# Optimization experiments

Hardware: AMD Instinct MI355X
Metric: run time of the kernel (lower is better)

## Reference

```python
import jax, jax.numpy as jnp
import numpy as np

B, T, C, H = 4, 4096, 1024, 16
HD = C // H  # 64


def setup_inputs() -> dict:
    key = jax.random.key(0)
    k1, k2, k3, k4 = jax.random.split(key, 4)
    x = jax.random.normal(k1, (B, T, C), dtype=jnp.float32)
    Wqkv = jax.random.normal(k2, (3 * C, C), dtype=jnp.float32) * (1.0 / np.sqrt(C))
    Wout = jax.random.normal(k3, (C, C), dtype=jnp.float32) * (1.0 / np.sqrt(C))
    bout = jax.random.normal(k4, (C,), dtype=jnp.float32) * 0.02
    return {"x": x, "Wqkv": Wqkv, "Wout": Wout, "bout": bout}


def reference(x, Wqkv, Wout, bout):
    # qkv projection (torch Linear: y = x @ W.T)
    qkv = x @ Wqkv.T                              # (B, T, 3C)
    qkv = qkv.reshape(B, T, H, 3 * HD)            # view(B, T, heads, 3*head_dim)
    q, k, v = jnp.split(qkv, 3, axis=-1)          # each (B, T, H, HD)
    # NOTE: faithful to source: q @ k.transpose(-2,-1) batches over (B,T)
    # and contracts head_dim -> attention over the HEADS axis, shape (B,T,H,H).
    att = jnp.einsum("bthd,btgd->bthg", q, k) / np.float32(np.sqrt(HD))
    att = jax.nn.softmax(att, axis=-1)            # softmax over heads axis g
    out = jnp.einsum("bthg,btgd->bthd", att, v)   # (B, T, H, HD)
    out = out.reshape(B, T, C)
    return out @ Wout.T + bout
```

## Files before the change

kernel.cpp:

```cpp
#include <hip/hip_runtime.h>
#include <hip/hip_bf16.h>
#include <stdint.h>

typedef __attribute__((ext_vector_type(8))) short bf16x8;
typedef __attribute__((ext_vector_type(4))) float f32x4;

__device__ __forceinline__ float b2f(unsigned short u) {
  union { unsigned u32; float f; } c; c.u32 = ((unsigned)u) << 16; return c.f;
}
__device__ __forceinline__ unsigned short f2b(float f) {
  union { float f; unsigned u; } c; c.f = f;
  unsigned u = c.u;
  return (unsigned short)((u + 0x7FFFu + ((u >> 16) & 1u)) >> 16);
}

__global__ __launch_bounds__(256) void cast_f32_bf16(const float* __restrict__ in,
                                                     unsigned short* __restrict__ out,
                                                     int n8) {
  int i = blockIdx.x * 256 + threadIdx.x;
  if (i >= n8) return;
  const float4* p = (const float4*)in + (size_t)i * 2;
  float4 a = p[0], b = p[1];
  union { bf16x8 v; unsigned short s[8]; } o;
  o.s[0] = f2b(a.x); o.s[1] = f2b(a.y); o.s[2] = f2b(a.z); o.s[3] = f2b(a.w);
  o.s[4] = f2b(b.x); o.s[5] = f2b(b.y); o.s[6] = f2b(b.z); o.s[7] = f2b(b.w);
  ((bf16x8*)out)[i] = o.v;
}

#define GLDS16(g, l)                                                          \
  __builtin_amdgcn_global_load_lds((const __attribute__((address_space(1))) void*)(g), \
                                   (__attribute__((address_space(3))) void*)(l), 16, 0, 0)

template <typename OutT, bool BIAS>
__global__ __launch_bounds__(256) void gemm_bt(const unsigned short* __restrict__ A,
                                               const unsigned short* __restrict__ B,
                                               OutT* __restrict__ C,
                                               const float* __restrict__ bias,
                                               int M, int N, int K) {
  __shared__ unsigned short As[128 * 32];
  __shared__ unsigned short Bs[128 * 32];
  const int tid  = threadIdx.x;
  const int lane = tid & 63;
  const int wave = tid >> 6;
  const int tileM = blockIdx.y * 128;
  const int tileN = blockIdx.x * 128;

  const int m_off = (wave >> 1) * 64;
  const int n_off = (wave & 1) * 64;

  f32x4 acc[4][4] = {};

  const int srow = tid >> 2;
  const int scol = (tid & 3) * 8;
  const unsigned short* gA = A + (size_t)(tileM + srow) * K + scol;
  const unsigned short* gB = B + (size_t)(tileN + srow) * K + scol;
  unsigned short* lA = &As[tid * 8];
  unsigned short* lB = &Bs[tid * 8];

  const int lr = lane & 15;
  const int lk = (lane >> 4) * 8;

  for (int k0 = 0; k0 < K; k0 += 32) {
    GLDS16(gA, lA);
    GLDS16(gA + (size_t)64 * K, lA + 2048);
    GLDS16(gB, lB);
    GLDS16(gB + (size_t)64 * K, lB + 2048);
    gA += 32; gB += 32;
    __syncthreads();

    bf16x8 af[4], bfr[4];
#pragma unroll
    for (int m = 0; m < 4; ++m)
      af[m] = *(const bf16x8*)&As[(m_off + m * 16 + lr) * 32 + lk];
#pragma unroll
    for (int n = 0; n < 4; ++n)
      bfr[n] = *(const bf16x8*)&Bs[(n_off + n * 16 + lr) * 32 + lk];

#pragma unroll
    for (int m = 0; m < 4; ++m)
#pragma unroll
      for (int n = 0; n < 4; ++n)
        acc[m][n] = __builtin_amdgcn_mfma_f32_16x16x32_bf16(af[m], bfr[n], acc[m][n], 0, 0, 0);
    __syncthreads();
  }

  const int crow0 = (lane >> 4) * 4;
  const int ccol  = lane & 15;
#pragma unroll
  for (int n = 0; n < 4; ++n) {
    const int col = tileN + n_off + n * 16 + ccol;
    float bv = 0.f;
    if (BIAS) bv = bias[col];
#pragma unroll
    for (int m = 0; m < 4; ++m) {
#pragma unroll
      for (int j = 0; j < 4; ++j) {
        const int row = tileM + m_off + m * 16 + crow0 + j;
        float v = acc[m][n][j] + bv;
        if constexpr (sizeof(OutT) == 2)
          ((unsigned short*)C)[(size_t)row * N + col] = f2b(v);
        else
          ((float*)C)[(size_t)row * N + col] = v;
      }
    }
  }
}

__global__ __launch_bounds__(256) void attn_heads(const unsigned short* __restrict__ qkv,
                                                  unsigned short* __restrict__ attout) {
  __shared__ float kvs[4][2][16 * 64];
  const int wave = threadIdx.x >> 6;
  const int lane = threadIdx.x & 63;
  const size_t tok = (size_t)blockIdx.x * 4 + wave;
  const int h = lane >> 2;
  const int s = lane & 3;

  const unsigned short* base = qkv + tok * 3072 + h * 192 + s * 16;
  bf16x8 q0 = *(const bf16x8*)(base);
  bf16x8 q1 = *(const bf16x8*)(base + 8);
  bf16x8 k0 = *(const bf16x8*)(base + 64);
  bf16x8 k1 = *(const bf16x8*)(base + 72);
  bf16x8 v0 = *(const bf16x8*)(base + 128);
  bf16x8 v1 = *(const bf16x8*)(base + 136);

  float q[16], kr[16], vr[16];
#pragma unroll
  for (int j = 0; j < 8; ++j) {
    q[j]      = b2f((unsigned short)q0[j]);
    q[8 + j]  = b2f((unsigned short)q1[j]);
    kr[j]     = b2f((unsigned short)k0[j]);
    kr[8 + j] = b2f((unsigned short)k1[j]);
    vr[j]     = b2f((unsigned short)v0[j]);
    vr[8 + j] = b2f((unsigned short)v1[j]);
  }

  float* kb = kvs[wave][0];
  float* vb = kvs[wave][1];
#pragma unroll
  for (int c = 0; c < 4; ++c) {
    const int off = h * 64 + (((s * 4 + c) * 4) ^ ((h & 7) << 2));
    *(float4*)&kb[off] = make_float4(kr[c * 4], kr[c * 4 + 1], kr[c * 4 + 2], kr[c * 4 + 3]);
    *(float4*)&vb[off] = make_float4(vr[c * 4], vr[c * 4 + 1], vr[c * 4 + 2], vr[c * 4 + 3]);
  }

  float att[16];
#pragma unroll
  for (int g = 0; g < 16; ++g) {
    float a = 0.f;
#pragma unroll
    for (int c = 0; c < 4; ++c) {
      const int off = g * 64 + (((s * 4 + c) * 4) ^ ((g & 7) << 2));
      float4 kf = *(const float4*)&kb[off];
      a += q[c * 4 + 0] * kf.x + q[c * 4 + 1] * kf.y +
           q[c * 4 + 2] * kf.z + q[c * 4 + 3] * kf.w;
    }
    a += __shfl_xor(a, 1);
    a += __shfl_xor(a, 2);
    att[g] = a * 0.125f;
  }

  float mx = att[0];
#pragma unroll
  for (int g = 1; g < 16; ++g) mx = fmaxf(mx, att[g]);
  float sum = 0.f;
#pragma unroll
  for (int g = 0; g < 16; ++g) { att[g] = __expf(att[g] - mx); sum += att[g]; }
  const float inv = 1.f / sum;

  float o[16];
#pragma unroll
  for (int j = 0; j < 16; ++j) o[j] = 0.f;
#pragma unroll
  for (int g = 0; g < 16; ++g) {
    const float pg = att[g];
#pragma unroll
    for (int c = 0; c < 4; ++c) {
      const int off = g * 64 + (((s * 4 + c) * 4) ^ ((g & 7) << 2));
      float4 vf = *(const float4*)&vb[off];
      o[c * 4 + 0] += pg * vf.x;
      o[c * 4 + 1] += pg * vf.y;
      o[c * 4 + 2] += pg * vf.z;
      o[c * 4 + 3] += pg * vf.w;
    }
  }

  union { bf16x8 v[2]; unsigned short u[16]; } ob;
#pragma unroll
  for (int j = 0; j < 16; ++j) ob.u[j] = f2b(o[j] * inv);
  bf16x8* dst = (bf16x8*)&attout[tok * 1024 + h * 64 + s * 16];
  dst[0] = ob.v[0];
  dst[1] = ob.v[1];
}

extern "C" void kernel_launch(void* const* d_in, const int* in_sizes, int n_in,
                              void* d_out, int out_size, void* d_ws, size_t ws_size,
                              hipStream_t stream) {
  const float* x    = (const float*)d_in[0];
  const float* Wqkv = (const float*)d_in[1];
  const float* Wout = (const float*)d_in[2];
  const float* bout = (const float*)d_in[3];
  float* out = (float*)d_out;

  char* ws = (char*)d_ws;
  unsigned short* xb     = (unsigned short*)(ws);
  unsigned short* wqkvb  = (unsigned short*)(ws + 33554432);
  unsigned short* woutb  = (unsigned short*)(ws + 39845888);
  unsigned short* qkv    = (unsigned short*)(ws + 41943040);
  unsigned short* attout = (unsigned short*)(ws + 142606336);

  cast_f32_bf16<<<8192, 256, 0, stream>>>(x, xb, 2097152);
  cast_f32_bf16<<<1536, 256, 0, stream>>>(Wqkv, wqkvb, 393216);
  cast_f32_bf16<<<512, 256, 0, stream>>>(Wout, woutb, 131072);

  gemm_bt<unsigned short, false><<<dim3(24, 128), 256, 0, stream>>>(
      xb, wqkvb, qkv, nullptr, 16384, 3072, 1024);

  attn_heads<<<4096, 256, 0, stream>>>(qkv, attout);

  gemm_bt<float, true><<<dim3(8, 128), 256, 0, stream>>>(
      attout, woutb, out, bout, 16384, 1024, 1024);
}
```

Measured before the change: 368.4 us.

## Replace GEMM with 256x256-tile, 8-wave, double-buffered pipelined kernel

Replaces the simple 128x128 GEMM, which had a single LDS buffer and two syncthreads per 32-wide k-step, with a 256x256 tile, 512-thread kernel. It uses a 64-wide k-step, double-buffered LDS with XOR swizzling, and staggered global-to-LDS prefetch interleaved with MFMA phases. Manual barriers, vmcnt waits and setprio are meant to overlap memory traffic with matrix math and avoid LDS bank conflicts. The larger tiles use much more LDS and registers, so occupancy drops, and the 1024x1024 output GEMM launches only 256 blocks.

New measurement: 346.2 us. 6.0% less time.

```diff
diff --git a/kernel.cpp b/kernel.cpp
--- a/kernel.cpp
+++ b/kernel.cpp
@@ -4,6 +4,7 @@
 
 typedef __attribute__((ext_vector_type(8))) short bf16x8;
 typedef __attribute__((ext_vector_type(4))) float f32x4;
+typedef unsigned short ushort_t;
 
 __device__ __forceinline__ float b2f(unsigned short u) {
   union { unsigned u32; float f; } c; c.u32 = ((unsigned)u) << 16; return c.f;
@@ -31,76 +32,135 @@
   __builtin_amdgcn_global_load_lds((const __attribute__((address_space(1))) void*)(g), \
                                    (__attribute__((address_space(3))) void*)(l), 16, 0, 0)
 
+#define BAR1()                                             \
+  __builtin_amdgcn_s_barrier();                            \
+  asm volatile("s_waitcnt lgkmcnt(0)" ::: "memory");       \
+  __builtin_amdgcn_sched_barrier(0)
+
+#define BAR2()                                             \
+  __builtin_amdgcn_sched_barrier(0);                       \
+  __builtin_amdgcn_s_barrier();                            \
+  asm volatile("" ::: "memory")
+
+#define VM4() asm volatile("s_waitcnt vmcnt(4)" ::: "memory")
+
 template <typename OutT, bool BIAS>
-__global__ __launch_bounds__(256) void gemm_bt(const unsigned short* __restrict__ A,
-                                               const unsigned short* __restrict__ B,
-                                               OutT* __restrict__ C,
-                                               const float* __restrict__ bias,
-                                               int M, int N, int K) {
-  __shared__ unsigned short As[128 * 32];
-  __shared__ unsigned short Bs[128 * 32];
+__global__ __launch_bounds__(512, 2) void gemm8p(const unsigned short* __restrict__ A,
+                                                 const unsigned short* __restrict__ B,
+                                                 OutT* __restrict__ C,
+                                                 const float* __restrict__ bias,
+                                                 int M, int N, int K) {
+  __shared__ ushort_t smA[2 * 16384];
+  __shared__ ushort_t smB[2 * 16384];
+
   const int tid  = threadIdx.x;
   const int lane = tid & 63;
   const int wave = tid >> 6;
-  const int tileM = blockIdx.y * 128;
-  const int tileN = blockIdx.x * 128;
-
-  const int m_off = (wave >> 1) * 64;
-  const int n_off = (wave & 1) * 64;
-
-  f32x4 acc[4][4] = {};
-
-  const int srow = tid >> 2;
-  const int scol = (tid & 3) * 8;
-  const unsigned short* gA = A + (size_t)(tileM + srow) * K + scol;
-  const unsigned short* gB = B + (size_t)(tileN + srow) * K + scol;
-  unsigned short* lA = &As[tid * 8];
-  unsigned short* lB = &Bs[tid * 8];
-
-  const int lr = lane & 15;
-  const int lk = (lane >> 4) * 8;
-
-  for (int k0 = 0; k0 < K; k0 += 32) {
-    GLDS16(gA, lA);
-    GLDS16(gA + (size_t)64 * K, lA + 2048);
-    GLDS16(gB, lB);
-    GLDS16(gB + (size_t)64 * K, lB + 2048);
-    gA += 32; gB += 32;
-    __syncthreads();
-
-    bf16x8 af[4], bfr[4];
-#pragma unroll
-    for (int m = 0; m < 4; ++m)
-      af[m] = *(const bf16x8*)&As[(m_off + m * 16 + lr) * 32 + lk];
-#pragma unroll
-    for (int n = 0; n < 4; ++n)
-      bfr[n] = *(const bf16x8*)&Bs[(n_off + n * 16 + lr) * 32 + lk];
-
-#pragma unroll
-    for (int m = 0; m < 4; ++m)
-#pragma unroll
-      for (int n = 0; n < 4; ++n)
-        acc[m][n] = __builtin_amdgcn_mfma_f32_16x16x32_bf16(af[m], bfr[n], acc[m][n], 0, 0, 0);
-    __syncthreads();
+  const int wm = wave >> 2;
+  const int wn = wave & 3;
+  const int tileM = blockIdx.y * 256;
+  const int tileN = blockIdx.x * 256;
+  const int NT = K >> 6;
+
+  const int srow = tid >> 3;
+  const int sg   = (tid & 7) ^ (srow & 7);
+  const unsigned short* Abase = A + (size_t)(tileM + srow) * K + sg * 8;
+  const unsigned short* Bbase = B + (size_t)(tileN + srow) * K + sg * 8;
+
+#define STAGE_A(h, tt, pp) {                                                   \
+    const unsigned short* s_ = Abase + (size_t)(h) * 128 * K + (size_t)(tt) * 64; \
+    GLDS16(s_, &smA[(pp) * 16384 + (h) * 8192 + tid * 8]);                     \
+    GLDS16(s_ + (size_t)64 * K, &smA[(pp) * 16384 + (h) * 8192 + 4096 + tid * 8]); }
+#define STAGE_B(h, tt, pp) {                                                   \
+    const unsigned short* s_ = Bbase + (size_t)(h) * 128 * K + (size_t)(tt) * 64; \
+    GLDS16(s_, &smB[(pp) * 16384 + (h) * 8192 + tid * 8]);                     \
+    GLDS16(s_ + (size_t)64 * K, &smB[(pp) * 16384 + (h) * 8192 + 4096 + tid * 8]); }
+
+  const int lr  = lane & 15;
+  const int kg  = lane >> 4;
+  const int gx0 = kg ^ (lr & 7);
+  const int gx1 = gx0 ^ 4;
+#define LDSA(pp, row, gx) (*(const bf16x8*)&smA[(pp) * 16384 + (row) * 64 + ((gx) << 3)])
+#define LDSB(pp, row, gx) (*(const bf16x8*)&smB[(pp) * 16384 + (row) * 64 + ((gx) << 3)])
+
+  f32x4 acc[8][4] = {};
+  bf16x8 af[4], bf[4];
+
+#define MFMA16(mh)                                                   \
+  __builtin_amdgcn_s_setprio(1);                                     \
+  _Pragma("unroll") for (int m = 0; m < 4; ++m)                      \
+    _Pragma("unroll") for (int n = 0; n < 4; ++n)                    \
+      acc[(mh) * 4 + m][n] =                                         \
+          __builtin_amdgcn_mfma_f32_16x16x32_bf16(af[m], bf[n], acc[(mh) * 4 + m][n], 0, 0, 0); \
+  __builtin_amdgcn_s_setprio(0)
+
+  STAGE_A(0, 0, 0); STAGE_A(1, 0, 0); STAGE_B(0, 0, 0); STAGE_B(1, 0, 0);
+  STAGE_A(0, 1, 1);
+  asm volatile("s_waitcnt vmcnt(2)" ::: "memory");
+  __builtin_amdgcn_s_barrier();
+  asm volatile("" ::: "memory");
+
+  const int arow0 = wm * 64 + lr;
+  const int brow0 = wn * 64 + lr;
+
+  for (int t = 0; t < NT; ++t) {
+    const int p  = t & 1;
+    const int pn = p ^ 1;
+    const bool s1 = (t + 1) < NT;
+    const bool s2 = (t + 2) < NT;
+
+#pragma unroll
+    for (int n = 0; n < 4; ++n) bf[n] = LDSB(p, brow0 + n * 16, gx0);
+#pragma unroll
+    for (int m = 0; m < 4; ++m) af[m] = LDSA(p, arow0 + m * 16, gx0);
+    if (s1) STAGE_B(0, t + 1, pn);
+    BAR1();
+    MFMA16(0);
+    VM4();
+    BAR2();
+
+#pragma unroll
+    for (int m = 0; m < 4; ++m) af[m] = LDSA(p, 128 + arow0 + m * 16, gx0);
+    if (s1) STAGE_B(1, t + 1, pn);
+    BAR1();
+    MFMA16(1);
+    BAR2();
+
+#pragma unroll
+    for (int n = 0; n < 4; ++n) bf[n] = LDSB(p, brow0 + n * 16, gx1);
+#pragma unroll
+    for (int m = 0; m < 4; ++m) af[m] = LDSA(p, arow0 + m * 16, gx1);
+    if (s1) STAGE_A(1, t + 1, pn);
+    BAR1();
+    MFMA16(0);
+    BAR2();
+
+#pragma unroll
+    for (int m = 0; m < 4; ++m) af[m] = LDSA(p, 128 + arow0 + m * 16, gx1);
+    if (s2) STAGE_A(0, t + 2, p);
+    BAR1();
+    MFMA16(1);
+    VM4();
+    BAR2();
   }
 
   const int crow0 = (lane >> 4) * 4;
   const int ccol  = lane & 15;
 #pragma unroll
   for (int n = 0; n < 4; ++n) {
-    const int col = tileN + n_off + n * 16 + ccol;
+    const int col = tileN + wn * 64 + n * 16 + ccol;
     float bv = 0.f;
     if (BIAS) bv = bias[col];
 #pragma unroll
-    for (int m = 0; m < 4; ++m) {
+    for (int m = 0; m < 8; ++m) {
+      const int row = tileM + (m >> 2) * 128 + wm * 64 + (m & 3) * 16 + crow0;
 #pragma unroll
       for (int j = 0; j < 4; ++j) {
-        const int row = tileM + m_off + m * 16 + crow0 + j;
         float v = acc[m][n][j] + bv;
         if constexpr (sizeof(OutT) == 2)
-          ((unsigned short*)C)[(size_t)row * N + col] = f2b(v);
+          ((unsigned short*)C)[(size_t)(row + j) * N + col] = f2b(v);
         else
-          ((float*)C)[(size_t)row * N + col] = v;
+          ((float*)C)[(size_t)(row + j) * N + col] = v;
       }
     }
   }
@@ -212,11 +272,11 @@
   cast_f32_bf16<<<1536, 256, 0, stream>>>(Wqkv, wqkvb, 393216);
   cast_f32_bf16<<<512, 256, 0, stream>>>(Wout, woutb, 131072);
 
-  gemm_bt<unsigned short, false><<<dim3(24, 128), 256, 0, stream>>>(
+  gemm8p<unsigned short, false><<<dim3(12, 64), 512, 0, stream>>>(
       xb, wqkvb, qkv, nullptr, 16384, 3072, 1024);
 
   attn_heads<<<4096, 256, 0, stream>>>(qkv, attout);
 
-  gemm_bt<float, true><<<dim3(8, 128), 256, 0, stream>>>(
+  gemm8p<float, true><<<dim3(4, 64), 512, 0, stream>>>(
       attout, woutb, out, bout, 16384, 1024, 1024);
 }
```
